# Kernel optimization log

Measured on AMD Instinct MI355X. Metric: run time of the kernel, lower is better.

The kernel has to match this reference:

```python
import jax, jax.numpy as jnp
import numpy as np

N = 50000          # nodes
E = 800000         # edges (avg in-degree 16)
NFEAT, F = 128, 64 # input feat, hidden width (outfeat = outd_1 = outd_2 = 64)
ALPHA = 0.2        # leaky relu slope
AVG_LIN = 16.0             # sum(bin*hist)/N for deg histogram (all deg 16)
AVG_LOG = float(np.log(17.0))  # sum(log(bin+1)*hist)/N


def setup_inputs():
    key = jax.random.key(0)
    ks = jax.random.split(key, 16)
    g = lambda i, shp, s: (jax.random.normal(ks[i], shp, jnp.float32) * s)
    return {
        "x": g(0, (N, NFEAT), 1.0),
        "adj": jnp.zeros((1,), jnp.float32),
        "edge_index": jax.random.randint(ks[1], (2, E), 0, N, dtype=jnp.int32),
        "W0": g(2, (NFEAT, F), NFEAT ** -0.5), "b0": jnp.zeros((F,), jnp.float32),
        "c1_pre_W": g(3, (2 * F, F), (2 * F) ** -0.5), "c1_pre_b": jnp.zeros((F,), jnp.float32),
        "c1_post_W": g(4, (5 * F, F), (5 * F) ** -0.5), "c1_post_b": jnp.zeros((F,), jnp.float32),
        "c1_lin_W": g(5, (F, F), F ** -0.5), "c1_lin_b": jnp.zeros((F,), jnp.float32),
        "c2_pre_W": g(6, (2 * F, F), (2 * F) ** -0.5), "c2_pre_b": jnp.zeros((F,), jnp.float32),
        "c2_post_W": g(7, (5 * F, F), (5 * F) ** -0.5), "c2_post_b": jnp.zeros((F,), jnp.float32),
        "c2_lin_W": g(8, (F, F), F ** -0.5), "c2_lin_b": jnp.zeros((F,), jnp.float32),
        "W2": g(9, (F, 1), F ** -0.5), "b2": jnp.zeros((1,), jnp.float32),
    }


def pna_conv(x, src, dst, pre_W, pre_b, post_W, post_b, lin_W, lin_b):
    # message: pre_nn(cat[x_i, x_j]) per edge  (x_i = target, x_j = source)
    h = jnp.concatenate([x[dst], x[src]], axis=-1) @ pre_W + pre_b  # [E, F]
    cnt = jax.ops.segment_sum(jnp.ones((h.shape[0],), h.dtype), dst, num_segments=N)
    deg = jnp.clip(cnt, 1.0)                                        # [N]
    mean = jax.ops.segment_sum(h, dst, num_segments=N) / deg[:, None]
    mx = jax.ops.segment_max(h, dst, num_segments=N)
    mx = jnp.where(cnt[:, None] > 0, mx, 0.0)                       # empty segs -> 0
    agg = jnp.concatenate([mean, mx], axis=-1)                      # [N, 2F]
    att = agg * (AVG_LOG / jnp.log(deg + 1.0))[:, None]             # attenuation scaler
    lin = agg * (deg / AVG_LIN)[:, None]                            # linear scaler
    out = jnp.concatenate([x, att, lin], axis=-1)                   # [N, 5F]
    out = out @ post_W + post_b
    return out @ lin_W + lin_b


def reference(x, adj, edge_index, W0, b0,
              c1_pre_W, c1_pre_b, c1_post_W, c1_post_b, c1_lin_W, c1_lin_b,
              c2_pre_W, c2_pre_b, c2_post_W, c2_post_b, c2_lin_W, c2_lin_b,
              W2, b2):
    src, dst = edge_index[0], edge_index[1]
    h = jax.nn.leaky_relu(x @ W0 + b0, negative_slope=ALPHA)  # dropout = id (eval)
    h = jax.nn.relu(pna_conv(h, src, dst, c1_pre_W, c1_pre_b, c1_post_W, c1_post_b, c1_lin_W, c1_lin_b))
    h = jax.nn.relu(pna_conv(h, src, dst, c2_pre_W, c2_pre_b, c2_post_W, c2_post_b, c2_lin_W, c2_lin_b))
    return h @ W2 + b2  # [N, 1]
```

## Files before the change

### kernel.cpp

```cpp
#include <hip/hip_runtime.h>
#include <hip/hip_bf16.h>

typedef __hip_bfloat16 bf16;
typedef unsigned short u16;
typedef unsigned int u32;
typedef __attribute__((ext_vector_type(8))) short short8;
typedef __attribute__((ext_vector_type(4))) float f32x4;

static constexpr float AVG_LOG_C = 2.8332133440562162f;
#define BCAP 2048
#define CHUNK 8192
#define PREP_TOTAL (8192 * 3 + 20480 * 2 + 64 * 6 + 1)

__device__ __forceinline__ u32 f2bf_bits(float f) {
    u32 u = __float_as_uint(f);
    return (u + 0x7fffu + ((u >> 16) & 1u)) >> 16;
}
__device__ __forceinline__ float bf2f(u16 b) {
    return __uint_as_float(((u32)b) << 16);
}

__global__ __launch_bounds__(1024) void detect_zero_kernel(
    const u32* __restrict__ xwords, int* __restrict__ flag,
    int* __restrict__ bcnt, int nb) {
    if (blockIdx.x == 0) {
        int tid = threadIdx.x;
        if (tid < 64) {
            int good = 0;
            for (int i = tid; i < 2048; i += 64) {
                u32 lo = xwords[i] & 0xffffu;
                float v = __uint_as_float(lo << 16);
                float a = fabsf(v);
                if (v == 0.0f || (a >= 1e-3f && a <= 100.0f)) good++;
            }
            for (int off = 32; off; off >>= 1) good += __shfl_xor(good, off, 64);
            if (tid == 0) *flag = (2 * good > 2048) ? 1 : 0;
        }
    } else {
        int i = (blockIdx.x - 1) * 1024 + threadIdx.x;
        if (i < nb) bcnt[i] = 0;
    }
}

__global__ __launch_bounds__(1024) void prep_scatter_kernel(
    const int* __restrict__ srcs, const int* __restrict__ dsts,
    int* __restrict__ bcnt, u32* __restrict__ bstage, int e, int nb,
    const void* __restrict__ W0r,  const void* __restrict__ b0r,
    const void* __restrict__ pre1r, const void* __restrict__ preb1r,
    const void* __restrict__ post1r, const void* __restrict__ postb1r,
    const void* __restrict__ lin1r, const void* __restrict__ linb1r,
    const void* __restrict__ pre2r, const void* __restrict__ preb2r,
    const void* __restrict__ post2r, const void* __restrict__ postb2r,
    const void* __restrict__ lin2r, const void* __restrict__ linb2r,
    const void* __restrict__ W2r,  const void* __restrict__ b2r,
    u16* __restrict__ W0p, u16* __restrict__ pre1p, u16* __restrict__ pre2p,
    u16* __restrict__ wf1p, u16* __restrict__ wf2p,
    float* __restrict__ bfo1, float* __restrict__ bfo2,
    float* __restrict__ preb1f, float* __restrict__ preb2f,
    float* __restrict__ b0f, float* __restrict__ W2f, float* __restrict__ b2f,
    const int* __restrict__ flag) {
    __shared__ int lhist[1024];
    __shared__ int lbase[1024];
    int tid = threadIdx.x;
    int scatB = (e + CHUNK - 1) / CHUNK;
    if ((int)blockIdx.x < scatB) {
        int cbase = blockIdx.x * CHUNK;
        for (int b = tid; b < nb; b += 1024) lhist[b] = 0;
        __syncthreads();
#pragma unroll
        for (int i = 0; i < CHUNK; i += 1024) {
            int e0 = cbase + i + tid;
            if (e0 < e) atomicAdd(&lhist[dsts[e0] >> 6], 1);
        }
        __syncthreads();
        for (int b = tid; b < nb; b += 1024) {
            int c = lhist[b];
            lbase[b] = c ? atomicAdd(&bcnt[b], c) : 0;
            lhist[b] = 0;
        }
        __syncthreads();
#pragma unroll
        for (int i = 0; i < CHUNK; i += 1024) {
            int e0 = cbase + i + tid;
            if (e0 < e) {
                int d = dsts[e0];
                int b = d >> 6;
                int pos = lbase[b] + atomicAdd(&lhist[b], 1);
                if (pos < BCAP)
                    bstage[(size_t)b * BCAP + pos] = (u32)srcs[e0] | ((u32)(d & 63) << 17);
            }
        }
        return;
    }
    int idx = ((int)blockIdx.x - scatB) * 1024 + tid;
    bool isbf = (*flag) != 0;
    auto ld = [&](const void* p, int i) -> float {
        return isbf ? bf2f(((const u16*)p)[i]) : ((const float*)p)[i];
    };
    if (idx < 8192) {
        int j = idx & 7, l = (idx >> 3) & 63, tt = idx >> 9;
        int c = tt & 3, s = tt >> 2;
        int kk = s * 32 + (l >> 4) * 8 + j;
        int col = c * 16 + (l & 15);
        W0p[idx] = (u16)f2bf_bits(ld(W0r, kk * 64 + col));
        return;
    }
    idx -= 8192;
    for (int which = 0; which < 2; ++which) {
        if (idx < 8192) {
            const void* src = which ? pre2r : pre1r;
            u16* dst = which ? pre2p : pre1p;
            int j = idx & 7, l = (idx >> 3) & 63, tt = idx >> 9;
            int c = tt & 7, s = tt >> 3;
            int kk = s * 32 + (l >> 4) * 8 + j;
            int col = c * 16 + (l & 15);
            float v = (col < 64) ? ld(src, kk * 64 + col)
                                 : ld(src, (64 + kk) * 64 + (col - 64));
            dst[idx] = (u16)f2bf_bits(v);
            return;
        }
        idx -= 8192;
    }
    for (int which = 0; which < 2; ++which) {
        if (idx < 20480) {
            const void* postW = which ? post2r : post1r;
            const void* linW  = which ? lin2r  : lin1r;
            u16* dst = which ? wf2p : wf1p;
            int j = idx & 7, l = (idx >> 3) & 63, tt = idx >> 9;
            int c = tt & 3, s = tt >> 2;
            int kk = s * 32 + (l >> 4) * 8 + j;
            int col = c * 16 + (l & 15);
            float a = 0.f;
            for (int k = 0; k < 64; ++k)
                a = fmaf(ld(postW, kk * 64 + k), ld(linW, k * 64 + col), a);
            dst[idx] = (u16)f2bf_bits(a);
            return;
        }
        idx -= 20480;
    }
    for (int which = 0; which < 2; ++which) {
        if (idx < 64) {
            const void* postb = which ? postb2r : postb1r;
            const void* linW  = which ? lin2r : lin1r;
            const void* linb  = which ? linb2r : linb1r;
            float* dst = which ? bfo2 : bfo1;
            float a = ld(linb, idx);
            for (int k = 0; k < 64; ++k)
                a = fmaf(ld(postb, k), ld(linW, k * 64 + idx), a);
            dst[idx] = a;
            return;
        }
        idx -= 64;
    }
    if (idx < 64) { preb1f[idx] = ld(preb1r, idx); return; }
    idx -= 64;
    if (idx < 64) { preb2f[idx] = ld(preb2r, idx); return; }
    idx -= 64;
    if (idx < 64) { b0f[idx] = ld(b0r, idx); return; }
    idx -= 64;
    if (idx < 64) { W2f[idx] = ld(W2r, idx); return; }
    idx -= 64;
    if (idx < 1) { b2f[0] = ld(b2r, 0); }
}

__global__ __launch_bounds__(1024) void gemm_x_pq_kernel(
    const void* __restrict__ xraw, const u16* __restrict__ W0p,
    const float* __restrict__ b0f, const u16* __restrict__ pre1p,
    u16* __restrict__ hA, u16* __restrict__ PQ,
    const int* __restrict__ flag, int n) {
    __shared__ __align__(16) u16 xsh[64 * 136];
    __shared__ __align__(16) u16 hsh[64 * 72];
    int tid = threadIdx.x;
    int wave = __builtin_amdgcn_readfirstlane(tid >> 6);
    int lane = tid & 63;
    int blockbase = blockIdx.x * 64;
    bool isbf = (*flag) != 0;
    {
        int row = tid >> 4;
        int cg = (tid & 15) * 8;
        int grow = blockbase + row;
        short8 v = short8{0, 0, 0, 0, 0, 0, 0, 0};
        if (grow < n) {
            if (isbf) {
                v = *(const short8*)((const u16*)xraw + (size_t)grow * 128 + cg);
            } else {
                const float* xf = (const float*)xraw + (size_t)grow * 128 + cg;
                f32x4 a0 = *(const f32x4*)xf;
                f32x4 a1 = *(const f32x4*)(xf + 4);
#pragma unroll
                for (int j = 0; j < 4; ++j) {
                    v[j]     = (short)f2bf_bits(a0[j]);
                    v[4 + j] = (short)f2bf_bits(a1[j]);
                }
            }
        }
        *(short8*)&xsh[row * 136 + cg] = v;
    }
    __syncthreads();
    int rt = wave & 3, ct = wave >> 2;
    int arl = rt * 16 + (lane & 15);
    int koff = (lane >> 4) * 8;
    f32x4 acc = f32x4{0.f, 0.f, 0.f, 0.f};
#pragma unroll
    for (int s = 0; s < 4; ++s) {
        short8 a = *(const short8*)&xsh[arl * 136 + s * 32 + koff];
        short8 b = *(const short8*)(W0p + ((size_t)(s * 4 + ct) * 64 + lane) * 8);
        acc = __builtin_amdgcn_mfma_f32_16x16x32_bf16(a, b, acc, 0, 0, 0);
    }
    {
        int col = ct * 16 + (lane & 15);
        float bv = b0f[col];
        int r0l = rt * 16 + (lane >> 4) * 4;
#pragma unroll
        for (int r = 0; r < 4; ++r) {
            float v = acc[r] + bv;
            v = v > 0.f ? v : 0.2f * v;
            u16 bits = (u16)f2bf_bits(v);
            hsh[(r0l + r) * 72 + col] = bits;
            int grow = blockbase + r0l + r;
            if (grow < n) hA[(size_t)grow * 64 + col] = bits;
        }
    }
    __syncthreads();
#pragma unroll
    for (int half = 0; half < 2; ++half) {
        int tile = wave * 2 + half;
        int rt2 = tile & 3, ct2 = tile >> 2;
        int ar2 = rt2 * 16 + (lane & 15);
        f32x4 acc2 = f32x4{0.f, 0.f, 0.f, 0.f};
#pragma unroll
        for (int s = 0; s < 2; ++s) {
            short8 a = *(const short8*)&hsh[ar2 * 72 + s * 32 + koff];
            short8 b = *(const short8*)(pre1p + ((size_t)(s * 8 + ct2) * 64 + lane) * 8);
            acc2 = __builtin_amdgcn_mfma_f32_16x16x32_bf16(a, b, acc2, 0, 0, 0);
        }
        int col2 = ct2 * 16 + (lane & 15);
        int r02 = rt2 * 16 + (lane >> 4) * 4;
#pragma unroll
        for (int r = 0; r < 4; ++r) {
            int grow = blockbase + r02 + r;
            if (grow < n) PQ[(size_t)grow * 128 + col2] = (u16)f2bf_bits(acc2[r]);
        }
    }
}

template<int FINAL>
__global__ __launch_bounds__(1024) void agg_gemm_kernel(
    const u16* __restrict__ PQ, const u16* __restrict__ h,
    const u32* __restrict__ bstage, const int* __restrict__ bcnt,
    const float* __restrict__ prebf, const u16* __restrict__ Wfp,
    const float* __restrict__ bfo, const u16* __restrict__ prenextp,
    u16* __restrict__ hout, u16* __restrict__ PQout,
    const float* __restrict__ W2f, const float* __restrict__ b2f,
    void* __restrict__ out, const int* __restrict__ flag, int n) {
    constexpr int PAD = 328;
    __shared__ __align__(16) u16 vsh[64 * PAD];
    __shared__ __align__(16) u16 hsh[64 * 72];
    __shared__ u32 lel[BCAP];
    __shared__ int loff[64], lcnt[64], lcur[64];
    __shared__ float fsum[64];
    int tid = threadIdx.x;
    int wave = __builtin_amdgcn_readfirstlane(tid >> 6);
    int lane = tid & 63;
    int b = blockIdx.x;
    int blockbase = b * 64;
    float pbl = prebf[lane];
    if (tid < 64) { lcnt[tid] = 0; if (FINAL) fsum[tid] = 0.f; }
    __syncthreads();
    int cb = min(bcnt[b], BCAP);
    const u32* st = bstage + (size_t)b * BCAP;
    for (int i = tid; i < cb; i += 1024) atomicAdd(&lcnt[st[i] >> 17], 1);
    __syncthreads();
    if (wave == 0) {
        int c = lcnt[lane];
        int s = c;
        for (int off = 1; off < 64; off <<= 1) {
            int t = __shfl_up(s, (unsigned)off, 64);
            if (lane >= off) s += t;
        }
        loff[lane] = s - c;
        lcur[lane] = s - c;
    }
    __syncthreads();
    for (int i = tid; i < cb; i += 1024) {
        u32 e = st[i];
        int pos = atomicAdd(&lcur[e >> 17], 1);
        lel[pos] = e & 0x1ffffu;
    }
    __syncthreads();
    const u16* Qb = PQ + 64 + lane;
#pragma unroll
    for (int t = 0; t < 4; ++t) {
        int nl = wave * 4 + t;
        int node = blockbase + nl;
        u16* vrow = &vsh[nl * PAD];
        if (node < n) {
            int beg = loff[nl], end = beg + lcnt[nl];
            int cnt = end - beg;
            float s = 0.f, m = -3.4e38f;
            int e = beg;
            for (; e + 8 <= end; e += 8) {
                float q0 = bf2f(Qb[(size_t)lel[e] * 128]);
                float q1 = bf2f(Qb[(size_t)lel[e + 1] * 128]);
                float q2 = bf2f(Qb[(size_t)lel[e + 2] * 128]);
                float q3 = bf2f(Qb[(size_t)lel[e + 3] * 128]);
                float q4 = bf2f(Qb[(size_t)lel[e + 4] * 128]);
                float q5 = bf2f(Qb[(size_t)lel[e + 5] * 128]);
                float q6 = bf2f(Qb[(size_t)lel[e + 6] * 128]);
                float q7 = bf2f(Qb[(size_t)lel[e + 7] * 128]);
                s += ((q0 + q1) + (q2 + q3)) + ((q4 + q5) + (q6 + q7));
                m = fmaxf(m, fmaxf(fmaxf(fmaxf(q0, q1), fmaxf(q2, q3)),
                                   fmaxf(fmaxf(q4, q5), fmaxf(q6, q7))));
            }
            for (; e + 4 <= end; e += 4) {
                float q0 = bf2f(Qb[(size_t)lel[e] * 128]);
                float q1 = bf2f(Qb[(size_t)lel[e + 1] * 128]);
                float q2 = bf2f(Qb[(size_t)lel[e + 2] * 128]);
                float q3 = bf2f(Qb[(size_t)lel[e + 3] * 128]);
                s += (q0 + q1) + (q2 + q3);
                m = fmaxf(fmaxf(m, fmaxf(q0, q1)), fmaxf(q2, q3));
            }
            for (; e < end; ++e) {
                float q = bf2f(Qb[(size_t)lel[e] * 128]);
                s += q;
                m = fmaxf(m, q);
            }
            float mean, mx, deg;
            if (cnt > 0) {
                deg = (float)cnt;
                float p = bf2f(PQ[(size_t)node * 128 + lane]) + pbl;
                mean = p + s / deg;
                mx = p + m;
            } else {
                deg = 1.f; mean = 0.f; mx = 0.f;
            }
            float att = AVG_LOG_C / logf(deg + 1.f);
            float lin = deg * (1.f / 16.f);
            vrow[lane]       = h[(size_t)node * 64 + lane];
            vrow[64 + lane]  = (u16)f2bf_bits(att * mean);
            vrow[128 + lane] = (u16)f2bf_bits(att * mx);
            vrow[192 + lane] = (u16)f2bf_bits(lin * mean);
            vrow[256 + lane] = (u16)f2bf_bits(lin * mx);
        } else {
            vrow[lane] = 0; vrow[64 + lane] = 0; vrow[128 + lane] = 0;
            vrow[192 + lane] = 0; vrow[256 + lane] = 0;
        }
    }
    __syncthreads();
    int rt = wave & 3, ct = wave >> 2;
    int arl = rt * 16 + (lane & 15);
    int koff = (lane >> 4) * 8;
    f32x4 acc = f32x4{0.f, 0.f, 0.f, 0.f};
#pragma unroll
    for (int s = 0; s < 10; ++s) {
        short8 a = *(const short8*)&vsh[arl * PAD + s * 32 + koff];
        short8 b2 = *(const short8*)(Wfp + ((size_t)(s * 4 + ct) * 64 + lane) * 8);
        acc = __builtin_amdgcn_mfma_f32_16x16x32_bf16(a, b2, acc, 0, 0, 0);
    }
    int col = ct * 16 + (lane & 15);
    float bv = bfo[col];
    int r0l = rt * 16 + (lane >> 4) * 4;
    if constexpr (!FINAL) {
#pragma unroll
        for (int r = 0; r < 4; ++r) {
            float v = fmaxf(acc[r] + bv, 0.f);
            u16 bits = (u16)f2bf_bits(v);
            hsh[(r0l + r) * 72 + col] = bits;
            int grow = blockbase + r0l + r;
            if (grow < n) hout[(size_t)grow * 64 + col] = bits;
        }
        __syncthreads();
#pragma unroll
        for (int half = 0; half < 2; ++half) {
            int tile = wave * 2 + half;
            int rt2 = tile & 3, ct2 = tile >> 2;
            int ar2 = rt2 * 16 + (lane & 15);
            f32x4 acc2 = f32x4{0.f, 0.f, 0.f, 0.f};
#pragma unroll
            for (int s = 0; s < 2; ++s) {
                short8 a = *(const short8*)&hsh[ar2 * 72 + s * 32 + koff];
                short8 b2 = *(const short8*)(prenextp + ((size_t)(s * 8 + ct2) * 64 + lane) * 8);
                acc2 = __builtin_amdgcn_mfma_f32_16x16x32_bf16(a, b2, acc2, 0, 0, 0);
            }
            int col2 = ct2 * 16 + (lane & 15);
            int r02 = rt2 * 16 + (lane >> 4) * 4;
#pragma unroll
            for (int r = 0; r < 4; ++r) {
                int grow = blockbase + r02 + r;
                if (grow < n) PQout[(size_t)grow * 128 + col2] = (u16)f2bf_bits(acc2[r]);
            }
        }
    } else {
        float w2 = W2f[col];
        float part[4];
#pragma unroll
        for (int r = 0; r < 4; ++r)
            part[r] = fmaxf(acc[r] + bv, 0.f) * w2;
#pragma unroll
        for (int r = 0; r < 4; ++r) {
            float v = part[r];
            v += __shfl_xor(v, 1, 64);
            v += __shfl_xor(v, 2, 64);
            v += __shfl_xor(v, 4, 64);
            v += __shfl_xor(v, 8, 64);
            if ((lane & 15) == 0) atomicAdd(&fsum[r0l + r], v);
        }
        __syncthreads();
        if (tid < 64) {
            int grow = blockbase + tid;
            if (grow < n) {
                float res = fsum[tid] + b2f[0];
                if (*flag) ((u16*)out)[grow] = (u16)f2bf_bits(res);
                else       ((float*)out)[grow] = res;
            }
        }
    }
}

extern "C" void kernel_launch(void* const* d_in, const int* in_sizes, int n_in,
                              void* d_out, int out_size, void* d_ws, size_t ws_size,
                              hipStream_t stream) {
    const int N = in_sizes[0] / 128;
    const int E = in_sizes[2] / 2;
    const int nb = (N + 63) >> 6;
    const int* ei = (const int*)d_in[2];
    const int* esrc = ei;
    const int* edst = ei + E;

    char* w = (char*)d_ws;
    auto alloc = [&](size_t bytes) -> void* {
        void* p = (void*)w;
        w += (bytes + 255) & ~(size_t)255;
        return p;
    };
    int* flag    = (int*)alloc(4);
    int* bcnt    = (int*)alloc((size_t)nb * 4);
    u32* bstage  = (u32*)alloc((size_t)nb * BCAP * 4);
    u16* W0p     = (u16*)alloc(128 * 64 * 2);
    u16* pre1p   = (u16*)alloc(64 * 128 * 2);
    u16* pre2p   = (u16*)alloc(64 * 128 * 2);
    u16* wf1p    = (u16*)alloc(320 * 64 * 2);
    u16* wf2p    = (u16*)alloc(320 * 64 * 2);
    float* bfo1  = (float*)alloc(64 * 4);
    float* bfo2  = (float*)alloc(64 * 4);
    float* preb1f= (float*)alloc(64 * 4);
    float* preb2f= (float*)alloc(64 * 4);
    float* b0f   = (float*)alloc(64 * 4);
    float* W2f   = (float*)alloc(64 * 4);
    float* b2f_  = (float*)alloc(4);
    u16* hA      = (u16*)alloc((size_t)N * 64 * 2);
    u16* hB      = (u16*)alloc((size_t)N * 64 * 2);
    u16* PQA     = (u16*)alloc((size_t)N * 128 * 2);
    u16* PQB     = (u16*)alloc((size_t)N * 128 * 2);

    detect_zero_kernel<<<1 + (nb + 1023) / 1024, 1024, 0, stream>>>(
        (const u32*)d_in[0], flag, bcnt, nb);

    int scatB = (E + CHUNK - 1) / CHUNK;
    int prepB = (PREP_TOTAL + 1023) / 1024;
    prep_scatter_kernel<<<scatB + prepB, 1024, 0, stream>>>(
        esrc, edst, bcnt, bstage, E, nb,
        d_in[3], d_in[4], d_in[5], d_in[6], d_in[7], d_in[8], d_in[9], d_in[10],
        d_in[11], d_in[12], d_in[13], d_in[14], d_in[15], d_in[16], d_in[17], d_in[18],
        W0p, pre1p, pre2p, wf1p, wf2p,
        bfo1, bfo2, preb1f, preb2f, b0f, W2f, b2f_, flag);

    int gblocks = (N + 63) / 64;
    gemm_x_pq_kernel<<<gblocks, 1024, 0, stream>>>(
        d_in[0], W0p, b0f, pre1p, hA, PQA, flag, N);

    agg_gemm_kernel<0><<<gblocks, 1024, 0, stream>>>(
        PQA, hA, bstage, bcnt, preb1f, wf1p, bfo1, pre2p, hB, PQB,
        nullptr, nullptr, nullptr, flag, N);

    agg_gemm_kernel<1><<<gblocks, 1024, 0, stream>>>(
        PQB, hB, bstage, bcnt, preb2f, wf2p, bfo2, nullptr, nullptr, nullptr,
        W2f, b2f_, d_out, flag, N);
}
```

Baseline: 203.1 us.

## Halve node-block size to 32 rows with 512-thread blocks and byte-offset gathers

```diff
diff --git a/kernel.cpp b/kernel.cpp
--- a/kernel.cpp
+++ b/kernel.cpp
@@ -8,8 +8,8 @@
 typedef __attribute__((ext_vector_type(4))) float f32x4;
 
 static constexpr float AVG_LOG_C = 2.8332133440562162f;
-#define BCAP 2048
-#define CHUNK 8192
+#define BCAP 1024
+#define CHUNK 4096
 #define PREP_TOTAL (8192 * 3 + 20480 * 2 + 64 * 6 + 1)
 
 __device__ __forceinline__ u32 f2bf_bits(float f) {
@@ -59,8 +59,8 @@
     float* __restrict__ preb1f, float* __restrict__ preb2f,
     float* __restrict__ b0f, float* __restrict__ W2f, float* __restrict__ b2f,
     const int* __restrict__ flag) {
-    __shared__ int lhist[1024];
-    __shared__ int lbase[1024];
+    __shared__ int lhist[2048];
+    __shared__ int lbase[2048];
     int tid = threadIdx.x;
     int scatB = (e + CHUNK - 1) / CHUNK;
     if ((int)blockIdx.x < scatB) {
@@ -70,7 +70,7 @@
 #pragma unroll
         for (int i = 0; i < CHUNK; i += 1024) {
             int e0 = cbase + i + tid;
-            if (e0 < e) atomicAdd(&lhist[dsts[e0] >> 6], 1);
+            if (e0 < e) atomicAdd(&lhist[dsts[e0] >> 5], 1);
         }
         __syncthreads();
         for (int b = tid; b < nb; b += 1024) {
@@ -84,10 +84,10 @@
             int e0 = cbase + i + tid;
             if (e0 < e) {
                 int d = dsts[e0];
-                int b = d >> 6;
+                int b = d >> 5;
                 int pos = lbase[b] + atomicAdd(&lhist[b], 1);
                 if (pos < BCAP)
-                    bstage[(size_t)b * BCAP + pos] = (u32)srcs[e0] | ((u32)(d & 63) << 17);
+                    bstage[(size_t)b * BCAP + pos] = (u32)srcs[e0] | ((u32)(d & 31) << 17);
             }
         }
         return;
@@ -163,17 +163,17 @@
     if (idx < 1) { b2f[0] = ld(b2r, 0); }
 }
 
-__global__ __launch_bounds__(1024) void gemm_x_pq_kernel(
+__global__ __launch_bounds__(512, 6) void gemm_x_pq_kernel(
     const void* __restrict__ xraw, const u16* __restrict__ W0p,
     const float* __restrict__ b0f, const u16* __restrict__ pre1p,
     u16* __restrict__ hA, u16* __restrict__ PQ,
     const int* __restrict__ flag, int n) {
-    __shared__ __align__(16) u16 xsh[64 * 136];
-    __shared__ __align__(16) u16 hsh[64 * 72];
+    __shared__ __align__(16) u16 xsh[32 * 136];
+    __shared__ __align__(16) u16 hsh[32 * 72];
     int tid = threadIdx.x;
     int wave = __builtin_amdgcn_readfirstlane(tid >> 6);
     int lane = tid & 63;
-    int blockbase = blockIdx.x * 64;
+    int blockbase = blockIdx.x * 32;
     bool isbf = (*flag) != 0;
     {
         int row = tid >> 4;
@@ -197,7 +197,7 @@
         *(short8*)&xsh[row * 136 + cg] = v;
     }
     __syncthreads();
-    int rt = wave & 3, ct = wave >> 2;
+    int rt = wave & 1, ct = wave >> 1;
     int arl = rt * 16 + (lane & 15);
     int koff = (lane >> 4) * 8;
     f32x4 acc = f32x4{0.f, 0.f, 0.f, 0.f};
@@ -225,7 +225,7 @@
 #pragma unroll
     for (int half = 0; half < 2; ++half) {
         int tile = wave * 2 + half;
-        int rt2 = tile & 3, ct2 = tile >> 2;
+        int rt2 = tile & 1, ct2 = tile >> 1;
         int ar2 = rt2 * 16 + (lane & 15);
         f32x4 acc2 = f32x4{0.f, 0.f, 0.f, 0.f};
 #pragma unroll
@@ -245,7 +245,7 @@
 }
 
 template<int FINAL>
-__global__ __launch_bounds__(1024) void agg_gemm_kernel(
+__global__ __launch_bounds__(512, 6) void agg_gemm_kernel(
     const u16* __restrict__ PQ, const u16* __restrict__ h,
     const u32* __restrict__ bstage, const int* __restrict__ bcnt,
     const float* __restrict__ prebf, const u16* __restrict__ Wfp,
@@ -254,41 +254,44 @@
     const float* __restrict__ W2f, const float* __restrict__ b2f,
     void* __restrict__ out, const int* __restrict__ flag, int n) {
     constexpr int PAD = 328;
-    __shared__ __align__(16) u16 vsh[64 * PAD];
-    __shared__ __align__(16) u16 hsh[64 * 72];
+    __shared__ __align__(16) u16 vsh[32 * PAD];
+    __shared__ __align__(16) u16 hsh[32 * 72];
     __shared__ u32 lel[BCAP];
-    __shared__ int loff[64], lcnt[64], lcur[64];
-    __shared__ float fsum[64];
+    __shared__ int loff[32], lcnt[32], lcur[32];
+    __shared__ float fsum[32];
     int tid = threadIdx.x;
     int wave = __builtin_amdgcn_readfirstlane(tid >> 6);
     int lane = tid & 63;
     int b = blockIdx.x;
-    int blockbase = b * 64;
+    int blockbase = b * 32;
     float pbl = prebf[lane];
-    if (tid < 64) { lcnt[tid] = 0; if (FINAL) fsum[tid] = 0.f; }
+    if (tid < 32) { lcnt[tid] = 0; if (FINAL) fsum[tid] = 0.f; }
     __syncthreads();
     int cb = min(bcnt[b], BCAP);
     const u32* st = bstage + (size_t)b * BCAP;
-    for (int i = tid; i < cb; i += 1024) atomicAdd(&lcnt[st[i] >> 17], 1);
+    for (int i = tid; i < cb; i += 512) atomicAdd(&lcnt[st[i] >> 17], 1);
     __syncthreads();
     if (wave == 0) {
-        int c = lcnt[lane];
+        int c = (lane < 32) ? lcnt[lane] : 0;
         int s = c;
-        for (int off = 1; off < 64; off <<= 1) {
+        for (int off = 1; off < 32; off <<= 1) {
             int t = __shfl_up(s, (unsigned)off, 64);
             if (lane >= off) s += t;
         }
-        loff[lane] = s - c;
-        lcur[lane] = s - c;
-    }
-    __syncthreads();
-    for (int i = tid; i < cb; i += 1024) {
+        if (lane < 32) {
+            loff[lane] = s - c;
+            lcur[lane] = s - c;
+        }
+    }
+    __syncthreads();
+    for (int i = tid; i < cb; i += 512) {
         u32 e = st[i];
         int pos = atomicAdd(&lcur[e >> 17], 1);
-        lel[pos] = e & 0x1ffffu;
-    }
-    __syncthreads();
-    const u16* Qb = PQ + 64 + lane;
+        lel[pos] = (e & 0x1ffffu) << 8;
+    }
+    __syncthreads();
+    const char* PQc = (const char*)PQ;
+    u32 voffb = 128u + 2u * (u32)lane;
 #pragma unroll
     for (int t = 0; t < 4; ++t) {
         int nl = wave * 4 + t;
@@ -300,28 +303,28 @@
             float s = 0.f, m = -3.4e38f;
             int e = beg;
             for (; e + 8 <= end; e += 8) {
-                float q0 = bf2f(Qb[(size_t)lel[e] * 128]);
-                float q1 = bf2f(Qb[(size_t)lel[e + 1] * 128]);
-                float q2 = bf2f(Qb[(size_t)lel[e + 2] * 128]);
-                float q3 = bf2f(Qb[(size_t)lel[e + 3] * 128]);
-                float q4 = bf2f(Qb[(size_t)lel[e + 4] * 128]);
-                float q5 = bf2f(Qb[(size_t)lel[e + 5] * 128]);
-                float q6 = bf2f(Qb[(size_t)lel[e + 6] * 128]);
-                float q7 = bf2f(Qb[(size_t)lel[e + 7] * 128]);
+                float q0 = bf2f(*(const u16*)(PQc + lel[e]     + voffb));
+                float q1 = bf2f(*(const u16*)(PQc + lel[e + 1] + voffb));
+                float q2 = bf2f(*(const u16*)(PQc + lel[e + 2] + voffb));
+                float q3 = bf2f(*(const u16*)(PQc + lel[e + 3] + voffb));
+                float q4 = bf2f(*(const u16*)(PQc + lel[e + 4] + voffb));
+                float q5 = bf2f(*(const u16*)(PQc + lel[e + 5] + voffb));
+                float q6 = bf2f(*(const u16*)(PQc + lel[e + 6] + voffb));
+                float q7 = bf2f(*(const u16*)(PQc + lel[e + 7] + voffb));
                 s += ((q0 + q1) + (q2 + q3)) + ((q4 + q5) + (q6 + q7));
                 m = fmaxf(m, fmaxf(fmaxf(fmaxf(q0, q1), fmaxf(q2, q3)),
                                    fmaxf(fmaxf(q4, q5), fmaxf(q6, q7))));
             }
             for (; e + 4 <= end; e += 4) {
-                float q0 = bf2f(Qb[(size_t)lel[e] * 128]);
-                float q1 = bf2f(Qb[(size_t)lel[e + 1] * 128]);
-                float q2 = bf2f(Qb[(size_t)lel[e + 2] * 128]);
-                float q3 = bf2f(Qb[(size_t)lel[e + 3] * 128]);
+                float q0 = bf2f(*(const u16*)(PQc + lel[e]     + voffb));
+                float q1 = bf2f(*(const u16*)(PQc + lel[e + 1] + voffb));
+                float q2 = bf2f(*(const u16*)(PQc + lel[e + 2] + voffb));
+                float q3 = bf2f(*(const u16*)(PQc + lel[e + 3] + voffb));
                 s += (q0 + q1) + (q2 + q3);
                 m = fmaxf(fmaxf(m, fmaxf(q0, q1)), fmaxf(q2, q3));
             }
             for (; e < end; ++e) {
-                float q = bf2f(Qb[(size_t)lel[e] * 128]);
+                float q = bf2f(*(const u16*)(PQc + lel[e] + voffb));
                 s += q;
                 m = fmaxf(m, q);
             }
@@ -347,7 +350,7 @@
         }
     }
     __syncthreads();
-    int rt = wave & 3, ct = wave >> 2;
+    int rt = wave & 1, ct = wave >> 1;
     int arl = rt * 16 + (lane & 15);
     int koff = (lane >> 4) * 8;
     f32x4 acc = f32x4{0.f, 0.f, 0.f, 0.f};
@@ -373,7 +376,7 @@
 #pragma unroll
         for (int half = 0; half < 2; ++half) {
             int tile = wave * 2 + half;
-            int rt2 = tile & 3, ct2 = tile >> 2;
+            int rt2 = tile & 1, ct2 = tile >> 1;
             int ar2 = rt2 * 16 + (lane & 15);
             f32x4 acc2 = f32x4{0.f, 0.f, 0.f, 0.f};
 #pragma unroll
@@ -406,7 +409,7 @@
             if ((lane & 15) == 0) atomicAdd(&fsum[r0l + r], v);
         }
         __syncthreads();
-        if (tid < 64) {
+        if (tid < 32) {
             int grow = blockbase + tid;
             if (grow < n) {
                 float res = fsum[tid] + b2f[0];
@@ -422,7 +425,7 @@
                               hipStream_t stream) {
     const int N = in_sizes[0] / 128;
     const int E = in_sizes[2] / 2;
-    const int nb = (N + 63) >> 6;
+    const int nb = (N + 31) >> 5;
     const int* ei = (const int*)d_in[2];
     const int* esrc = ei;
     const int* edst = ei + E;
@@ -465,15 +468,15 @@
         W0p, pre1p, pre2p, wf1p, wf2p,
         bfo1, bfo2, preb1f, preb2f, b0f, W2f, b2f_, flag);
 
-    int gblocks = (N + 63) / 64;
-    gemm_x_pq_kernel<<<gblocks, 1024, 0, stream>>>(
+    int gblocks = (N + 31) / 32;
+    gemm_x_pq_kernel<<<gblocks, 512, 0, stream>>>(
         d_in[0], W0p, b0f, pre1p, hA, PQA, flag, N);
 
-    agg_gemm_kernel<0><<<gblocks, 1024, 0, stream>>>(
+    agg_gemm_kernel<0><<<gblocks, 512, 0, stream>>>(
         PQA, hA, bstage, bcnt, preb1f, wf1p, bfo1, pre2p, hB, PQB,
         nullptr, nullptr, nullptr, flag, N);
 
-    agg_gemm_kernel<1><<<gblocks, 1024, 0, stream>>>(
+    agg_gemm_kernel<1><<<gblocks, 512, 0, stream>>>(
         PQB, hB, bstage, bcnt, preb2f, wf2p, bfo2, nullptr, nullptr, nullptr,
         W2f, b2f_, d_out, flag, N);
 }
```

Result: no change. 204.6 us (+0.7%).

## Merge edge scatter, weight prep and first GEMM into one launch

Applied to the files above, without the earlier changes.

```diff
diff --git a/kernel.cpp b/kernel.cpp
--- a/kernel.cpp
+++ b/kernel.cpp
@@ -1,7 +1,6 @@
 #include <hip/hip_runtime.h>
 #include <hip/hip_bf16.h>
 
-typedef __hip_bfloat16 bf16;
 typedef unsigned short u16;
 typedef unsigned int u32;
 typedef __attribute__((ext_vector_type(8))) short short8;
@@ -10,7 +9,7 @@
 static constexpr float AVG_LOG_C = 2.8332133440562162f;
 #define BCAP 2048
 #define CHUNK 8192
-#define PREP_TOTAL (8192 * 3 + 20480 * 2 + 64 * 6 + 1)
+#define PREP2_TOTAL (8192 + 20480 * 2 + 128)
 
 __device__ __forceinline__ u32 f2bf_bits(float f) {
     u32 u = __float_as_uint(f);
@@ -20,83 +19,53 @@
     return __uint_as_float(((u32)b) << 16);
 }
 
-__global__ __launch_bounds__(1024) void detect_zero_kernel(
-    const u32* __restrict__ xwords, int* __restrict__ flag,
-    int* __restrict__ bcnt, int nb) {
-    if (blockIdx.x == 0) {
-        int tid = threadIdx.x;
-        if (tid < 64) {
-            int good = 0;
-            for (int i = tid; i < 2048; i += 64) {
-                u32 lo = xwords[i] & 0xffffu;
-                float v = __uint_as_float(lo << 16);
-                float a = fabsf(v);
-                if (v == 0.0f || (a >= 1e-3f && a <= 100.0f)) good++;
-            }
-            for (int off = 32; off; off >>= 1) good += __shfl_xor(good, off, 64);
-            if (tid == 0) *flag = (2 * good > 2048) ? 1 : 0;
-        }
-    } else {
-        int i = (blockIdx.x - 1) * 1024 + threadIdx.x;
+__device__ __forceinline__ bool block_detect(const u32* __restrict__ xwords,
+                                             int* sflag, int tid) {
+    if (tid < 64) {
+        int good = 0;
+        for (int i = tid; i < 2048; i += 64) {
+            u32 lo = xwords[i] & 0xffffu;
+            float v = __uint_as_float(lo << 16);
+            float a = fabsf(v);
+            if (v == 0.0f || (a >= 1e-3f && a <= 100.0f)) good++;
+        }
+        for (int off = 32; off; off >>= 1) good += __shfl_xor(good, off, 64);
+        if (tid == 0) *sflag = (2 * good > 2048) ? 1 : 0;
+    }
+    __syncthreads();
+    return *sflag != 0;
+}
+
+__global__ __launch_bounds__(512) void k0_kernel(
+    const u32* __restrict__ xwords, int* __restrict__ flag, int* __restrict__ bcnt,
+    const void* __restrict__ W0r, const void* __restrict__ b0r,
+    const void* __restrict__ pre1r, const void* __restrict__ preb1r,
+    const void* __restrict__ preb2r, const void* __restrict__ W2r,
+    const void* __restrict__ b2r,
+    u16* __restrict__ W0p, u16* __restrict__ pre1p,
+    float* __restrict__ b0f, float* __restrict__ preb1f,
+    float* __restrict__ preb2f, float* __restrict__ W2f, float* __restrict__ b2f,
+    int nb, int zB) {
+    __shared__ int sflag;
+    int tid = threadIdx.x;
+    int bx = (int)blockIdx.x;
+    if (bx == 0) {
+        bool v = block_detect(xwords, &sflag, tid);
+        if (tid == 0) *flag = v ? 1 : 0;
+        return;
+    }
+    bx -= 1;
+    if (bx < zB) {
+        int i = bx * 512 + tid;
         if (i < nb) bcnt[i] = 0;
-    }
-}
-
-__global__ __launch_bounds__(1024) void prep_scatter_kernel(
-    const int* __restrict__ srcs, const int* __restrict__ dsts,
-    int* __restrict__ bcnt, u32* __restrict__ bstage, int e, int nb,
-    const void* __restrict__ W0r,  const void* __restrict__ b0r,
-    const void* __restrict__ pre1r, const void* __restrict__ preb1r,
-    const void* __restrict__ post1r, const void* __restrict__ postb1r,
-    const void* __restrict__ lin1r, const void* __restrict__ linb1r,
-    const void* __restrict__ pre2r, const void* __restrict__ preb2r,
-    const void* __restrict__ post2r, const void* __restrict__ postb2r,
-    const void* __restrict__ lin2r, const void* __restrict__ linb2r,
-    const void* __restrict__ W2r,  const void* __restrict__ b2r,
-    u16* __restrict__ W0p, u16* __restrict__ pre1p, u16* __restrict__ pre2p,
-    u16* __restrict__ wf1p, u16* __restrict__ wf2p,
-    float* __restrict__ bfo1, float* __restrict__ bfo2,
-    float* __restrict__ preb1f, float* __restrict__ preb2f,
-    float* __restrict__ b0f, float* __restrict__ W2f, float* __restrict__ b2f,
-    const int* __restrict__ flag) {
-    __shared__ int lhist[1024];
-    __shared__ int lbase[1024];
-    int tid = threadIdx.x;
-    int scatB = (e + CHUNK - 1) / CHUNK;
-    if ((int)blockIdx.x < scatB) {
-        int cbase = blockIdx.x * CHUNK;
-        for (int b = tid; b < nb; b += 1024) lhist[b] = 0;
-        __syncthreads();
-#pragma unroll
-        for (int i = 0; i < CHUNK; i += 1024) {
-            int e0 = cbase + i + tid;
-            if (e0 < e) atomicAdd(&lhist[dsts[e0] >> 6], 1);
-        }
-        __syncthreads();
-        for (int b = tid; b < nb; b += 1024) {
-            int c = lhist[b];
-            lbase[b] = c ? atomicAdd(&bcnt[b], c) : 0;
-            lhist[b] = 0;
-        }
-        __syncthreads();
-#pragma unroll
-        for (int i = 0; i < CHUNK; i += 1024) {
-            int e0 = cbase + i + tid;
-            if (e0 < e) {
-                int d = dsts[e0];
-                int b = d >> 6;
-                int pos = lbase[b] + atomicAdd(&lhist[b], 1);
-                if (pos < BCAP)
-                    bstage[(size_t)b * BCAP + pos] = (u32)srcs[e0] | ((u32)(d & 63) << 17);
-            }
-        }
         return;
     }
-    int idx = ((int)blockIdx.x - scatB) * 1024 + tid;
-    bool isbf = (*flag) != 0;
+    bx -= zB;
+    bool isbf = block_detect(xwords, &sflag, tid);
     auto ld = [&](const void* p, int i) -> float {
         return isbf ? bf2f(((const u16*)p)[i]) : ((const float*)p)[i];
     };
+    int idx = bx * 512 + tid;
     if (idx < 8192) {
         int j = idx & 7, l = (idx >> 3) & 63, tt = idx >> 9;
         int c = tt & 3, s = tt >> 2;
@@ -106,74 +75,148 @@
         return;
     }
     idx -= 8192;
-    for (int which = 0; which < 2; ++which) {
+    if (idx < 8192) {
+        int j = idx & 7, l = (idx >> 3) & 63, tt = idx >> 9;
+        int c = tt & 7, s = tt >> 3;
+        int kk = s * 32 + (l >> 4) * 8 + j;
+        int col = c * 16 + (l & 15);
+        float v = (col < 64) ? ld(pre1r, kk * 64 + col)
+                             : ld(pre1r, (64 + kk) * 64 + (col - 64));
+        pre1p[idx] = (u16)f2bf_bits(v);
+        return;
+    }
+    idx -= 8192;
+    if (idx < 64) { b0f[idx] = ld(b0r, idx); return; }
+    idx -= 64;
+    if (idx < 64) { preb1f[idx] = ld(preb1r, idx); return; }
+    idx -= 64;
+    if (idx < 64) { preb2f[idx] = ld(preb2r, idx); return; }
+    idx -= 64;
+    if (idx < 64) { W2f[idx] = ld(W2r, idx); return; }
+    idx -= 64;
+    if (idx < 1) { b2f[0] = ld(b2r, 0); }
+}
+
+__global__ __launch_bounds__(1024) void k1_kernel(
+    const void* __restrict__ xraw,
+    const int* __restrict__ srcs, const int* __restrict__ dsts,
+    int* __restrict__ bcnt, u32* __restrict__ bstage,
+    const u16* __restrict__ W0p, const u16* __restrict__ pre1p,
+    const float* __restrict__ b0f,
+    const void* __restrict__ pre2r,
+    const void* __restrict__ post1r, const void* __restrict__ postb1r,
+    const void* __restrict__ lin1r, const void* __restrict__ linb1r,
+    const void* __restrict__ post2r, const void* __restrict__ postb2r,
+    const void* __restrict__ lin2r, const void* __restrict__ linb2r,
+    u16* __restrict__ pre2p, u16* __restrict__ wf1p, u16* __restrict__ wf2p,
+    float* __restrict__ bfo1, float* __restrict__ bfo2,
+    const int* __restrict__ flag,
+    u16* __restrict__ hA, u16* __restrict__ PQ,
+    int n, int e, int nb, int scatB, int prepB) {
+    __shared__ union {
+        struct { int lhist[2048]; int lbase[2048]; } sc;
+        struct { __align__(16) u16 xsh[64 * 136]; __align__(16) u16 hsh[64 * 72]; } gx;
+    } sm;
+    int tid = threadIdx.x;
+    int bx = (int)blockIdx.x;
+
+    if (bx < scatB) {
+        int cbase = bx * CHUNK;
+        for (int b = tid; b < nb; b += 1024) sm.sc.lhist[b] = 0;
+        __syncthreads();
+#pragma unroll
+        for (int i = 0; i < CHUNK; i += 1024) {
+            int e0 = cbase + i + tid;
+            if (e0 < e) atomicAdd(&sm.sc.lhist[dsts[e0] >> 6], 1);
+        }
+        __syncthreads();
+        for (int b = tid; b < nb; b += 1024) {
+            int c = sm.sc.lhist[b];
+            sm.sc.lbase[b] = c ? atomicAdd(&bcnt[b], c) : 0;
+            sm.sc.lhist[b] = 0;
+        }
+        __syncthreads();
+#pragma unroll
+        for (int i = 0; i < CHUNK; i += 1024) {
+            int e0 = cbase + i + tid;
+            if (e0 < e) {
+                int d = dsts[e0];
+                int b = d >> 6;
+                int pos = sm.sc.lbase[b] + atomicAdd(&sm.sc.lhist[b], 1);
+                if (pos < BCAP)
+                    bstage[(size_t)b * BCAP + pos] = (u32)srcs[e0] | ((u32)(d & 63) << 17);
+            }
+        }
+        return;
+    }
+    bx -= scatB;
+
+    if (bx < prepB) {
+        bool isbf = (*flag) != 0;
+        auto ld = [&](const void* p, int i) -> float {
+            return isbf ? bf2f(((const u16*)p)[i]) : ((const float*)p)[i];
+        };
+        int idx = bx * 1024 + tid;
         if (idx < 8192) {
-            const void* src = which ? pre2r : pre1r;
-            u16* dst = which ? pre2p : pre1p;
             int j = idx & 7, l = (idx >> 3) & 63, tt = idx >> 9;
             int c = tt & 7, s = tt >> 3;
             int kk = s * 32 + (l >> 4) * 8 + j;
             int col = c * 16 + (l & 15);
-            float v = (col < 64) ? ld(src, kk * 64 + col)
-                                 : ld(src, (64 + kk) * 64 + (col - 64));
-            dst[idx] = (u16)f2bf_bits(v);
+            float v = (col < 64) ? ld(pre2r, kk * 64 + col)
+                                 : ld(pre2r, (64 + kk) * 64 + (col - 64));
+            pre2p[idx] = (u16)f2bf_bits(v);
             return;
         }
         idx -= 8192;
-    }
-    for (int which = 0; which < 2; ++which) {
-        if (idx < 20480) {
-            const void* postW = which ? post2r : post1r;
-            const void* linW  = which ? lin2r  : lin1r;
-            u16* dst = which ? wf2p : wf1p;
-            int j = idx & 7, l = (idx >> 3) & 63, tt = idx >> 9;
-            int c = tt & 3, s = tt >> 2;
-            int kk = s * 32 + (l >> 4) * 8 + j;
-            int col = c * 16 + (l & 15);
-            float a = 0.f;
-            for (int k = 0; k < 64; ++k)
-                a = fmaf(ld(postW, kk * 64 + k), ld(linW, k * 64 + col), a);
-            dst[idx] = (u16)f2bf_bits(a);
-            return;
-        }
-        idx -= 20480;
-    }
-    for (int which = 0; which < 2; ++which) {
-        if (idx < 64) {
-            const void* postb = which ? postb2r : postb1r;
-            const void* linW  = which ? lin2r : lin1r;
-            const void* linb  = which ? linb2r : linb1r;
-            float* dst = which ? bfo2 : bfo1;
-            float a = ld(linb, idx);
-            for (int k = 0; k < 64; ++k)
-                a = fmaf(ld(postb, k), ld(linW, k * 64 + idx), a);
-            dst[idx] = a;
-            return;
-        }
-        idx -= 64;
-    }
-    if (idx < 64) { preb1f[idx] = ld(preb1r, idx); return; }
-    idx -= 64;
-    if (idx < 64) { preb2f[idx] = ld(preb2r, idx); return; }
-    idx -= 64;
-    if (idx < 64) { b0f[idx] = ld(b0r, idx); return; }
-    idx -= 64;
-    if (idx < 64) { W2f[idx] = ld(W2r, idx); return; }
-    idx -= 64;
-    if (idx < 1) { b2f[0] = ld(b2r, 0); }
-}
-
-__global__ __launch_bounds__(1024) void gemm_x_pq_kernel(
-    const void* __restrict__ xraw, const u16* __restrict__ W0p,
-    const float* __restrict__ b0f, const u16* __restrict__ pre1p,
-    u16* __restrict__ hA, u16* __restrict__ PQ,
-    const int* __restrict__ flag, int n) {
-    __shared__ __align__(16) u16 xsh[64 * 136];
-    __shared__ __align__(16) u16 hsh[64 * 72];
-    int tid = threadIdx.x;
+        for (int which = 0; which < 2; ++which) {
+            if (idx < 20480) {
+                const void* postW = which ? post2r : post1r;
+                const void* linW  = which ? lin2r  : lin1r;
+                u16* dst = which ? wf2p : wf1p;
+                int j = idx & 7, l = (idx >> 3) & 63, tt = idx >> 9;
+                int c = tt & 3, s = tt >> 2;
+                int kk = s * 32 + (l >> 4) * 8 + j;
+                int col = c * 16 + (l & 15);
+                float a = 0.f;
+                if (isbf) {
+                    const u16* pw = (const u16*)postW + (size_t)kk * 64;
+                    const u16* lw = (const u16*)linW + col;
+#pragma unroll 8
+                    for (int k = 0; k < 64; ++k)
+                        a = fmaf(bf2f(pw[k]), bf2f(lw[(size_t)k * 64]), a);
+                } else {
+                    const float* pw = (const float*)postW + (size_t)kk * 64;
+                    const float* lw = (const float*)linW + col;
+#pragma unroll 8
+                    for (int k = 0; k < 64; ++k)
+                        a = fmaf(pw[k], lw[(size_t)k * 64], a);
+                }
+                dst[idx] = (u16)f2bf_bits(a);
+                return;
+            }
+            idx -= 20480;
+        }
+        for (int which = 0; which < 2; ++which) {
+            if (idx < 64) {
+                const void* postb = which ? postb2r : postb1r;
+                const void* linW  = which ? lin2r : lin1r;
+                const void* linb  = which ? linb2r : linb1r;
+                float* dst = which ? bfo2 : bfo1;
+                float a = ld(linb, idx);
+                for (int k = 0; k < 64; ++k)
+                    a = fmaf(ld(postb, k), ld(linW, k * 64 + idx), a);
+                dst[idx] = a;
+                return;
+            }
+            idx -= 64;
+        }
+        return;
+    }
+    bx -= prepB;
+
     int wave = __builtin_amdgcn_readfirstlane(tid >> 6);
     int lane = tid & 63;
-    int blockbase = blockIdx.x * 64;
+    int blockbase = bx * 64;
     bool isbf = (*flag) != 0;
     {
         int row = tid >> 4;
@@ -194,7 +237,7 @@
                 }
             }
         }
-        *(short8*)&xsh[row * 136 + cg] = v;
+        *(short8*)&sm.gx.xsh[row * 136 + cg] = v;
     }
     __syncthreads();
     int rt = wave & 3, ct = wave >> 2;
@@ -203,7 +246,7 @@
     f32x4 acc = f32x4{0.f, 0.f, 0.f, 0.f};
 #pragma unroll
     for (int s = 0; s < 4; ++s) {
-        short8 a = *(const short8*)&xsh[arl * 136 + s * 32 + koff];
+        short8 a = *(const short8*)&sm.gx.xsh[arl * 136 + s * 32 + koff];
         short8 b = *(const short8*)(W0p + ((size_t)(s * 4 + ct) * 64 + lane) * 8);
         acc = __builtin_amdgcn_mfma_f32_16x16x32_bf16(a, b, acc, 0, 0, 0);
     }
@@ -216,7 +259,7 @@
             float v = acc[r] + bv;
             v = v > 0.f ? v : 0.2f * v;
             u16 bits = (u16)f2bf_bits(v);
-            hsh[(r0l + r) * 72 + col] = bits;
+            sm.gx.hsh[(r0l + r) * 72 + col] = bits;
             int grow = blockbase + r0l + r;
             if (grow < n) hA[(size_t)grow * 64 + col] = bits;
         }
@@ -230,7 +273,7 @@
         f32x4 acc2 = f32x4{0.f, 0.f, 0.f, 0.f};
 #pragma unroll
         for (int s = 0; s < 2; ++s) {
-            short8 a = *(const short8*)&hsh[ar2 * 72 + s * 32 + koff];
+            short8 a = *(const short8*)&sm.gx.hsh[ar2 * 72 + s * 32 + koff];
             short8 b = *(const short8*)(pre1p + ((size_t)(s * 8 + ct2) * 64 + lane) * 8);
             acc2 = __builtin_amdgcn_mfma_f32_16x16x32_bf16(a, b, acc2, 0, 0, 0);
         }
@@ -453,27 +496,28 @@
     u16* PQA     = (u16*)alloc((size_t)N * 128 * 2);
     u16* PQB     = (u16*)alloc((size_t)N * 128 * 2);
 
-    detect_zero_kernel<<<1 + (nb + 1023) / 1024, 1024, 0, stream>>>(
-        (const u32*)d_in[0], flag, bcnt, nb);
-
+    int zB = (nb + 511) / 512;
+    k0_kernel<<<1 + zB + 33, 512, 0, stream>>>(
+        (const u32*)d_in[0], flag, bcnt,
+        d_in[3], d_in[4], d_in[5], d_in[6], d_in[12], d_in[17], d_in[18],
+        W0p, pre1p, b0f, preb1f, preb2f, W2f, b2f_, nb, zB);
+
+    int gB = (N + 63) / 64;
     int scatB = (E + CHUNK - 1) / CHUNK;
-    int prepB = (PREP_TOTAL + 1023) / 1024;
-    prep_scatter_kernel<<<scatB + prepB, 1024, 0, stream>>>(
-        esrc, edst, bcnt, bstage, E, nb,
-        d_in[3], d_in[4], d_in[5], d_in[6], d_in[7], d_in[8], d_in[9], d_in[10],
-        d_in[11], d_in[12], d_in[13], d_in[14], d_in[15], d_in[16], d_in[17], d_in[18],
-        W0p, pre1p, pre2p, wf1p, wf2p,
-        bfo1, bfo2, preb1f, preb2f, b0f, W2f, b2f_, flag);
-
-    int gblocks = (N + 63) / 64;
-    gemm_x_pq_kernel<<<gblocks, 1024, 0, stream>>>(
-        d_in[0], W0p, b0f, pre1p, hA, PQA, flag, N);
-
-    agg_gemm_kernel<0><<<gblocks, 1024, 0, stream>>>(
+    int prepB = (PREP2_TOTAL + 1023) / 1024;
+    k1_kernel<<<scatB + prepB + gB, 1024, 0, stream>>>(
+        d_in[0], esrc, edst, bcnt, bstage,
+        W0p, pre1p, b0f,
+        d_in[11], d_in[7], d_in[8], d_in[9], d_in[10],
+        d_in[13], d_in[14], d_in[15], d_in[16],
+        pre2p, wf1p, wf2p, bfo1, bfo2, flag,
+        hA, PQA, N, E, nb, scatB, prepB);
+
+    agg_gemm_kernel<0><<<gB, 1024, 0, stream>>>(
         PQA, hA, bstage, bcnt, preb1f, wf1p, bfo1, pre2p, hB, PQB,
         nullptr, nullptr, nullptr, flag, N);
 
-    agg_gemm_kernel<1><<<gblocks, 1024, 0, stream>>>(
+    agg_gemm_kernel<1><<<gB, 1024, 0, stream>>>(
         PQB, hB, bstage, bcnt, preb2f, wf2p, bfo2, nullptr, nullptr, nullptr,
         W2f, b2f_, d_out, flag, N);
 }
```

New measurement: 194.5 us (median of 2 runs). 1.04x faster.
